# Performance work log

Measured on AMD Instinct MI355X. Metric: run time of the kernel, lower is better.

## Reference

```python
import jax, jax.numpy as jnp
import numpy as np

N_NODES = 100000
N_EDGES = 1000000
IN_FEATS = 128
HIDDEN = 256


def setup_inputs() -> dict:
    key = jax.random.key(0)
    ks = jax.random.split(key, 8)
    h_src_nodes = jax.random.normal(ks[0], (N_NODES, IN_FEATS), dtype=jnp.float32)
    h_dst_nodes = jax.random.normal(ks[1], (N_NODES, IN_FEATS), dtype=jnp.float32)
    src = jax.random.randint(ks[2], (N_EDGES,), 0, N_NODES, dtype=jnp.int32)
    dst = jax.random.randint(ks[3], (N_EDGES,), 0, N_NODES, dtype=jnp.int32)
    # MLP params, stored as [in, out] so forward is x @ W + b
    s1 = 1.0 / np.sqrt(2 * IN_FEATS)
    s2 = 1.0 / np.sqrt(HIDDEN)
    W1 = jax.random.uniform(ks[4], (2 * IN_FEATS, HIDDEN), jnp.float32, -s1, s1)
    b1 = jax.random.uniform(ks[5], (HIDDEN,), jnp.float32, -s1, s1)
    W2 = jax.random.uniform(ks[6], (HIDDEN, 1), jnp.float32, -s2, s2)
    b2 = jax.random.uniform(ks[7], (1,), jnp.float32, -s2, s2)
    return {"h_src_nodes": h_src_nodes, "h_dst_nodes": h_dst_nodes,
            "src": src, "dst": dst, "W1": W1, "b1": b1, "W2": W2, "b2": b2}


def reference(h_src_nodes, h_dst_nodes, src, dst, W1, b1, W2, b2):
    # gather endpoint features per edge, concat -> [E, 2*in_feats]
    h_cat = jnp.concatenate([h_src_nodes[src], h_dst_nodes[dst]], axis=1)
    hidden = jax.nn.relu(h_cat @ W1 + b1)        # [E, hidden]
    score = (hidden @ W2 + b2).squeeze(-1)        # [E]
    return score
```

## Files before the change

### kernel.cpp

```cpp
#include <hip/hip_runtime.h>
#include <hip/hip_bf16.h>
#include <stdint.h>

#define IN_FEATS 128
#define HID 256
#define BM 64
#define LDA 136

typedef __bf16   bf16x4 __attribute__((ext_vector_type(4)));
typedef __bf16   bf16x8 __attribute__((ext_vector_type(8)));
typedef float    f32x4  __attribute__((ext_vector_type(4)));
typedef _Float16 h2     __attribute__((ext_vector_type(2)));
typedef _Float16 h8     __attribute__((ext_vector_type(8)));

__global__ void k_prep(const float* __restrict__ W1, const float* __restrict__ W2,
                       __bf16* __restrict__ W1P, _Float16* __restrict__ W2H) {
    int t = blockIdx.x * 256 + threadIdx.x;
    if (t < 8192) {
        int lane  = t & 63;
        int nblk  = (t >> 6) & 15;
        int ks    = (t >> 10) & 3;
        int which = (t >> 12) & 1;
        int qr = lane & 15, qg = lane >> 4;
        int n  = nblk * 16 + qr;
        int k0 = which * 128 + ks * 32 + qg * 8;
        bf16x8 v;
#pragma unroll
        for (int j = 0; j < 8; ++j)
            v[j] = (__bf16)W1[(size_t)(k0 + j) * HID + n];
        *(bf16x8*)(W1P + (size_t)t * 8) = v;
    } else {
        int i = t - 8192;
        if (i < HID) W2H[i] = (_Float16)W2[i];
    }
}

__global__ __launch_bounds__(256) void k_proj(
    const float* __restrict__ hs, const float* __restrict__ hd,
    const __bf16* __restrict__ W1P, const float* __restrict__ b1,
    _Float16* __restrict__ Ps, _Float16* __restrict__ Pd, int NN)
{
    __shared__ __bf16 Atile[BM][LDA];

    const int which = blockIdx.y;
    const float* __restrict__ h = which ? hd : hs;
    _Float16* __restrict__ P = which ? Pd : Ps;

    const int lane  = threadIdx.x & 63;
    const int w     = threadIdx.x >> 6;
    const int n0    = w * 64;
    const int node0 = blockIdx.x * BM;
    const int qr = lane & 15;
    const int qg = lane >> 4;
    const bf16x8* __restrict__ W1Pv = (const bf16x8*)W1P;

    {
        const int t = threadIdx.x;
#pragma unroll
        for (int j = 0; j < 8; ++j) {
            int g   = t + 256 * j;
            int row = g >> 5;
            int c4  = (g & 31) * 4;
            int rsrc = node0 + row; if (rsrc > NN - 1) rsrc = NN - 1;
            float4 f = *(const float4*)(h + (size_t)rsrc * IN_FEATS + c4);
            bf16x4 v = { (__bf16)f.x, (__bf16)f.y, (__bf16)f.z, (__bf16)f.w };
            *(bf16x4*)&Atile[row][c4] = v;
        }
    }
    __syncthreads();

    f32x4 acc[4][4];
#pragma unroll
    for (int m = 0; m < 4; ++m)
#pragma unroll
        for (int n = 0; n < 4; ++n) acc[m][n] = (f32x4){0.f, 0.f, 0.f, 0.f};

#pragma unroll
    for (int ks = 0; ks < 4; ++ks) {
        bf16x8 a[4];
#pragma unroll
        for (int m = 0; m < 4; ++m)
            a[m] = *(const bf16x8*)&Atile[m * 16 + qr][ks * 32 + qg * 8];
#pragma unroll
        for (int n = 0; n < 4; ++n) {
            bf16x8 b = W1Pv[((size_t)(which * 4 + ks) * 16 + w * 4 + n) * 64 + lane];
#pragma unroll
            for (int m = 0; m < 4; ++m)
                acc[m][n] = __builtin_amdgcn_mfma_f32_16x16x32_bf16(a[m], b, acc[m][n], 0, 0, 0);
        }
    }

    const bool even = (qr & 1) == 0;
    const int i0 = even ? 0 : 2;
#pragma unroll
    for (int n = 0; n < 4; ++n) {
        const int col = n0 + n * 16 + qr;
        const float bias = which ? 0.f : b1[col];
#pragma unroll
        for (int m = 0; m < 4; ++m) {
            const int rowb = m * 16 + qg * 4;
            float v[4], o[4];
#pragma unroll
            for (int i = 0; i < 4; ++i) {
                v[i] = acc[m][n][i] + bias;
                o[i] = __shfl_xor(v[i], 1, 64);
            }
#pragma unroll
            for (int i = 0; i < 2; ++i) {
                const int r = i0 + i;
                if (node0 + rowb + r < NN) {
                    auto pk = even ? __builtin_amdgcn_cvt_pkrtz(v[r], o[r])
                                   : __builtin_amdgcn_cvt_pkrtz(o[r], v[r]);
                    *(unsigned*)(P + (size_t)(node0 + rowb + r) * HID + (col & ~1)) =
                        __builtin_bit_cast(unsigned, pk);
                }
            }
        }
    }
}

__device__ __forceinline__ float dot8f(h8 a, h8 c, h8 w, float acc) {
    h8 r = a + c;
    r = __builtin_elementwise_max(r, (h8)(_Float16)0.f);
#pragma unroll
    for (int j = 0; j < 4; ++j) {
        h2 p = {r[2 * j], r[2 * j + 1]};
        h2 q = {w[2 * j], w[2 * j + 1]};
        acc = __builtin_amdgcn_fdot2(p, q, acc, false);
    }
    return acc;
}

__global__ __launch_bounds__(256) void k_edge(
    const _Float16* __restrict__ Ps, const _Float16* __restrict__ Pd,
    const int* __restrict__ src, const int* __restrict__ dst,
    const _Float16* __restrict__ W2H, const float* __restrict__ b2,
    float* __restrict__ out, int e_beg, int e_end)
{
    const int lane = threadIdx.x & 63;
    const int q = lane & 15;
    const int g = lane >> 4;
    const int wave = blockIdx.x * 4 + (threadIdx.x >> 6);
    const int nw = gridDim.x * 4;

    const h8* __restrict__ W2v = (const h8*)W2H;
    const h8 wa0 = W2v[q];
    const h8 wa1 = W2v[16 + q];
    const float bias = b2[0];

    for (int base = e_beg + wave * 8; base < e_end; base += nw * 8) {
        const int e0 = base + g;
        const int e1 = base + 4 + g;
        const bool v0 = (e0 < e_end), v1 = (e1 < e_end);
        float acc0 = 0.f, acc1 = 0.f;
        if (v0) {
            const h8* ps = (const h8*)(Ps + (size_t)src[e0] * HID);
            const h8* pd = (const h8*)(Pd + (size_t)dst[e0] * HID);
            h8 a0 = ps[q], a1 = ps[16 + q], c0 = pd[q], c1 = pd[16 + q];
            if (v1) {
                const h8* ps1 = (const h8*)(Ps + (size_t)src[e1] * HID);
                const h8* pd1 = (const h8*)(Pd + (size_t)dst[e1] * HID);
                h8 b0 = ps1[q], b1v = ps1[16 + q], d0 = pd1[q], d1 = pd1[16 + q];
                acc0 = dot8f(a0, c0, wa0, acc0);
                acc0 = dot8f(a1, c1, wa1, acc0);
                acc1 = dot8f(b0, d0, wa0, acc1);
                acc1 = dot8f(b1v, d1, wa1, acc1);
            } else {
                acc0 = dot8f(a0, c0, wa0, acc0);
                acc0 = dot8f(a1, c1, wa1, acc0);
            }
        }
#pragma unroll
        for (int m = 1; m < 16; m <<= 1) {
            acc0 += __shfl_xor(acc0, m, 64);
            acc1 += __shfl_xor(acc1, m, 64);
        }
        if (q == 0) {
            if (v0) out[e0] = acc0 + bias;
            if (v1) out[e1] = acc1 + bias;
        }
    }
}

extern "C" void kernel_launch(void* const* d_in, const int* in_sizes, int n_in,
                              void* d_out, int out_size, void* d_ws, size_t ws_size,
                              hipStream_t stream) {
    const float* h_src = (const float*)d_in[0];
    const float* h_dst = (const float*)d_in[1];
    const int*   src   = (const int*)d_in[2];
    const int*   dst   = (const int*)d_in[3];
    const float* W1    = (const float*)d_in[4];
    const float* b1    = (const float*)d_in[5];
    const float* W2    = (const float*)d_in[6];
    const float* b2    = (const float*)d_in[7];
    float* out = (float*)d_out;

    const int E  = in_sizes[2];
    const int NN = in_sizes[0] / IN_FEATS;

    __bf16*    W1P = (__bf16*)d_ws;
    _Float16*  W2H = (_Float16*)((char*)d_ws + 131072);
    _Float16*  Ps  = (_Float16*)((char*)d_ws + 262144);
    _Float16*  Pd  = Ps + (size_t)NN * HID;

    k_prep<<<33, 256, 0, stream>>>(W1, W2, W1P, W2H);
    dim3 gA((NN + BM - 1) / BM, 2);
    k_proj<<<gA, 256, 0, stream>>>(h_src, h_dst, W1P, b1, Ps, Pd, NN);
    const int Eh = E / 2;
    k_edge<<<2048, 256, 0, stream>>>(Ps, Pd, src, dst, W2H, b2, out, 0, Eh);
    k_edge<<<2048, 256, 0, stream>>>(Ps, Pd, src, dst, W2H, b2, out, Eh, E);
}
```

Baseline: 313.9 us.

## Permute hidden columns for vectorized projection stores and merge edge launches

The projection epilogue now writes each lane's four n-block accumulators as one 8-byte packed store. This places hidden columns in a permuted order, which removes the cross-lane shuffles and replaces many 4-byte stores with fewer wider ones. W2 is permuted the same way in the prep kernel, so the edge dot product stays correct. The two half-range edge kernel launches are merged into a single launch over all edges, saving one launch and its tail.

```diff
diff --git a/kernel.cpp b/kernel.cpp
--- a/kernel.cpp
+++ b/kernel.cpp
@@ -31,7 +31,10 @@
         *(bf16x8*)(W1P + (size_t)t * 8) = v;
     } else {
         int i = t - 8192;
-        if (i < HID) W2H[i] = (_Float16)W2[i];
+        if (i < HID) {
+            int w = i >> 6, r = (i >> 2) & 15, n = i & 3;
+            W2H[i] = (_Float16)W2[w * 64 + n * 16 + r];
+        }
     }
 }
 
@@ -90,30 +93,24 @@
         }
     }
 
-    const bool even = (qr & 1) == 0;
-    const int i0 = even ? 0 : 2;
-#pragma unroll
-    for (int n = 0; n < 4; ++n) {
-        const int col = n0 + n * 16 + qr;
-        const float bias = which ? 0.f : b1[col];
-#pragma unroll
-        for (int m = 0; m < 4; ++m) {
-            const int rowb = m * 16 + qg * 4;
-            float v[4], o[4];
-#pragma unroll
-            for (int i = 0; i < 4; ++i) {
-                v[i] = acc[m][n][i] + bias;
-                o[i] = __shfl_xor(v[i], 1, 64);
-            }
-#pragma unroll
-            for (int i = 0; i < 2; ++i) {
-                const int r = i0 + i;
-                if (node0 + rowb + r < NN) {
-                    auto pk = even ? __builtin_amdgcn_cvt_pkrtz(v[r], o[r])
-                                   : __builtin_amdgcn_cvt_pkrtz(o[r], v[r]);
-                    *(unsigned*)(P + (size_t)(node0 + rowb + r) * HID + (col & ~1)) =
-                        __builtin_bit_cast(unsigned, pk);
-                }
+    float bias[4];
+#pragma unroll
+    for (int n = 0; n < 4; ++n)
+        bias[n] = which ? 0.f : b1[n0 + n * 16 + qr];
+
+#pragma unroll
+    for (int m = 0; m < 4; ++m) {
+#pragma unroll
+        for (int i = 0; i < 4; ++i) {
+            const int row = node0 + m * 16 + qg * 4 + i;
+            if (row < NN) {
+                auto p0 = __builtin_amdgcn_cvt_pkrtz(acc[m][0][i] + bias[0],
+                                                     acc[m][1][i] + bias[1]);
+                auto p1 = __builtin_amdgcn_cvt_pkrtz(acc[m][2][i] + bias[2],
+                                                     acc[m][3][i] + bias[3]);
+                uint2 wd = { __builtin_bit_cast(unsigned, p0),
+                             __builtin_bit_cast(unsigned, p1) };
+                *(uint2*)(P + (size_t)row * HID + n0 + qr * 4) = wd;
             }
         }
     }
@@ -135,7 +132,7 @@
     const _Float16* __restrict__ Ps, const _Float16* __restrict__ Pd,
     const int* __restrict__ src, const int* __restrict__ dst,
     const _Float16* __restrict__ W2H, const float* __restrict__ b2,
-    float* __restrict__ out, int e_beg, int e_end)
+    float* __restrict__ out, int E)
 {
     const int lane = threadIdx.x & 63;
     const int q = lane & 15;
@@ -148,10 +145,10 @@
     const h8 wa1 = W2v[16 + q];
     const float bias = b2[0];
 
-    for (int base = e_beg + wave * 8; base < e_end; base += nw * 8) {
+    for (int base = wave * 8; base < E; base += nw * 8) {
         const int e0 = base + g;
         const int e1 = base + 4 + g;
-        const bool v0 = (e0 < e_end), v1 = (e1 < e_end);
+        const bool v0 = (e0 < E), v1 = (e1 < E);
         float acc0 = 0.f, acc1 = 0.f;
         if (v0) {
             const h8* ps = (const h8*)(Ps + (size_t)src[e0] * HID);
@@ -206,7 +203,5 @@
     k_prep<<<33, 256, 0, stream>>>(W1, W2, W1P, W2H);
     dim3 gA((NN + BM - 1) / BM, 2);
     k_proj<<<gA, 256, 0, stream>>>(h_src, h_dst, W1P, b1, Ps, Pd, NN);
-    const int Eh = E / 2;
-    k_edge<<<2048, 256, 0, stream>>>(Ps, Pd, src, dst, W2H, b2, out, 0, Eh);
-    k_edge<<<2048, 256, 0, stream>>>(Ps, Pd, src, dst, W2H, b2, out, Eh, E);
-}
+    k_edge<<<2048, 256, 0, stream>>>(Ps, Pd, src, dst, W2H, b2, out, E);
+}
```

After: 298.8 us. 4.8% less time.
